# Kernel tuning notes

Hardware: AMD Instinct MI355X
Metric: run time of the kernel (lower is better)

The kernel has to match this reference:

```python
import jax, jax.numpy as jnp
import numpy as np

B = 256; L = 512; PRED = 96; DVARS = 21
P = 16; STRIDE = 16
N = (L - P) // STRIDE + 1      # 32 patches
DM = P * P                     # d_model = 256
K = 5                          # DctAtt low-freq coeffs
EPS_BN = 1e-5


def _dct_mats(n_len):
    # torch_dct DCT-II / DCT-III as dense matrices (exact same scaling as torch_dct)
    n = jnp.arange(n_len, dtype=jnp.float32)
    C = jnp.cos(jnp.pi * (2.0 * n[None, :] + 1.0) * n[:, None] / (2.0 * n_len))  # (k, m)
    D2 = 2.0 * C                                  # dct(x, norm=None):  X = x @ D2.T
    w0 = jnp.where(n == 0, 0.5, 1.0)
    D3 = (C.T * w0[None, :]) / n_len              # idct(X, norm=None): x = X @ D3.T
    rL = jnp.sqrt(jnp.asarray(n_len, jnp.float32))
    s_ortho = jnp.where(n == 0, 0.5 / rL, 0.5 * jnp.sqrt(2.0) / rL)  # unnorm -> ortho scale
    return D2, D3, s_ortho


def _bn(x, g, b):
    # BatchNorm1d, training-mode batch stats (biased var), x: (B, C, Lc)
    m = jnp.mean(x, axis=(0, 2), keepdims=True)
    v = jnp.var(x, axis=(0, 2), keepdims=True)
    return g[None, :, None] * (x - m) * jax.lax.rsqrt(v + EPS_BN) + b[None, :, None]


def _gelu(x):
    return jax.nn.gelu(x, approximate=False)  # torch nn.GELU default = exact erf


def setup_inputs():
    key = jax.random.key(0)
    ks = jax.random.split(key, 24)
    r = lambda i, shp, s=0.02: jax.random.normal(ks[i], shp, jnp.float32) * s
    return dict(
        x=jax.random.normal(ks[0], (B, L, DVARS), jnp.float32),
        w_dct=r(1, (DVARS,), 0.2), b_dct=r(2, (DVARS,), 0.02),
        W_embed=r(3, (P, DM), 0.05), b_embed=r(4, (DM,), 0.02),
        W_linres=r(5, (N * DM, PRED), 0.01), b_linres=r(6, (PRED,), 0.02),
        W_dres=r(7, (DM, P), 0.05), b_dres=r(8, (P,), 0.02),
        w_dc=r(9, (N, P), 0.1), b_dc=r(10, (N,), 0.02),
        w_dc1=r(11, (N, 3), 0.2), b_dc1=r(12, (N,), 0.02),
        g_dctnorm=jnp.ones((DVARS,), jnp.float32), b_dctnorm=jnp.zeros((DVARS,), jnp.float32),
        g_patchnorm=jnp.ones((N,), jnp.float32), b_patchnorm=jnp.zeros((N,), jnp.float32),
        g_depthnorm=jnp.ones((N,), jnp.float32), b_depthnorm=jnp.zeros((N,), jnp.float32),
        thr_p=jnp.array([0.3], jnp.float32),
        W_m1=r(13, (L, PRED), 0.02), b_m1=r(14, (PRED,), 0.02),
        W_m2=r(15, (PRED, PRED), 0.05), b_m2=r(16, (PRED,), 0.02),
        a_dw_w=r(17, (K,), 0.2), a_dw_b=r(18, (), 0.02),
        a_cw=jnp.float32(1.0) + r(19, (), 0.1), a_cb=r(20, (), 0.02),
        a_g=jnp.ones((), jnp.float32), a_b=jnp.zeros((), jnp.float32),
    )


def reference(x, w_dct, b_dct, W_embed, b_embed, W_linres, b_linres,
              W_dres, b_dres, w_dc, b_dc, w_dc1, b_dc1,
              g_dctnorm, b_dctnorm, g_patchnorm, b_patchnorm,
              g_depthnorm, b_depthnorm, thr_p,
              W_m1, b_m1, W_m2, b_m2,
              a_dw_w, a_dw_b, a_cw, a_cb, a_g, a_b):
    Bx = x.shape[0]
    D2, D3, s_ortho = _dct_mats(L)
    xT = jnp.transpose(x, (0, 2, 1))                       # (B,D,L)
    # dctConv = depthwise 1x1 conv => per-channel scale+bias (same layer reused twice)
    x_res = xT * w_dct[:, None] + b_dct[:, None]
    z_dct = xT @ D2.T                                      # dct(norm=None)
    # adaptive_high_freq_mask
    energy = jnp.sum(z_dct * z_dct, axis=-1)               # (B,D)
    med = jnp.median(energy, axis=1, keepdims=True)
    norm_e = energy / (med + 1e-6)
    thr = jnp.quantile(norm_e, thr_p[0])                   # global quantile over all elems
    mask = (norm_e > thr).astype(x.dtype)[..., None]       # broadcasts over freq axis
    z = (z_dct * mask) * w_dct[:, None] + b_dct[:, None]
    z = _gelu(z)
    z = _bn(z, g_dctnorm, b_dctnorm)
    z1 = z @ D3.T + x_res                                  # idct + residual, (B,D,L)
    # patchify (unfold)
    idx = jnp.arange(N)[:, None] * STRIDE + jnp.arange(P)[None, :]
    zp = xT[..., idx].reshape(Bx * DVARS, N, P)            # (BD,N,P)
    z_p = zp @ W_embed + b_embed                           # (BD,N,DM)
    z_res = jnp.transpose(z_p.reshape(Bx, DVARS, N * DM) @ W_linres + b_linres, (0, 2, 1))
    res = z_p @ W_dres + b_dres                            # (BD,N,P)
    # depth_conv: depthwise conv, kernel=P, stride=P over DM=P*P
    zd = jnp.einsum('bnqp,np->bnq', z_p.reshape(Bx * DVARS, N, P, P), w_dc) + b_dc[:, None]
    zd = _bn(zd + res, g_patchnorm, b_patchnorm)
    z2 = _gelu(zd)
    # depth_conv1: depthwise k=3 pad=1
    zpad = jnp.pad(z2, ((0, 0), (0, 0), (1, 1)))
    zc = (w_dc1[:, 0, None] * zpad[..., :-2] + w_dc1[:, 1, None] * zpad[..., 1:-1]
          + w_dc1[:, 2, None] * zpad[..., 2:]) + b_dc1[:, None]
    zc = _bn(zc, g_depthnorm, b_depthnorm)
    zc = _gelu(zc) + z2
    z2f = zc.reshape(Bx, DVARS, N * P)                     # (B,D,L)
    # DctAtt on z1*z2f (low-freq pick + dwConv(k=5,stride=5) + BN(1) + GELU + 1x1 + softmax)
    prod = z1 * z2f
    low = (prod @ D2.T[:, :K]) * s_ortho[:K]               # ortho DCT, first K coeffs (B,D,K)
    att = low @ a_dw_w + a_dw_b                            # (B,D)
    m = jnp.mean(att); v = jnp.var(att)
    att = a_g * (att - m) * jax.lax.rsqrt(v + EPS_BN) + a_b
    att = _gelu(att)
    att1 = jax.nn.softmax(att * a_cw + a_cb, axis=-1)[..., None]  # (B,D,1)
    zsum = z1 * att1 + z2f * (1.0 - att1)
    z_mlp = _gelu(zsum @ W_m1 + b_m1) @ W_m2 + b_m2        # Mlp, (B,D,PRED)
    return z_res + jnp.transpose(z_mlp, (0, 2, 1))         # (B,PRED,D)
```

## Files before the change

### kernel.cpp

```cpp
#include <hip/hip_runtime.h>
#include <hip/hip_bf16.h>

#define B_    256
#define L_    512
#define DV    21
#define NROW  5376
#define NP    32
#define PP    16
#define PRED_ 96

static const size_t OFF_XT    = 0;
static const size_t OFF_ZA    = 2752512;
static const size_t OFF_Z1    = 5505024;
static const size_t OFF_ZCP   = 8257536;
static const size_t OFF_D2    = 11010048;
static const size_t OFF_D3    = 11272192;
static const size_t OFF_M     = 11534336;
static const size_t OFF_TN    = 11583488;
static const size_t OFF_TB    = 11591680;
static const size_t OFF_C     = 11592192;
static const size_t OFF_EN    = 11592320;
static const size_t OFF_NORM  = 11597696;
static const size_t OFF_ATT   = 11603072;
static const size_t OFF_ATT1  = 11608448;
static const size_t OFF_STAT  = 11613824;
static const size_t OFF_ABD   = 11614080;
static const size_t OFF_ABP   = 11614144;
static const size_t OFF_ABDEP = 11614208;
static const size_t OFF_FLAG  = 11614272;
static const size_t OFF_STG   = 11614336;

static const int S_WDCT=0, S_BDCT=24, S_WE=48, S_BE=4144, S_WL=4400, S_BL=790832,
  S_WD=790928, S_BDRES=795024, S_WDC=795040, S_BDC=795552, S_WDC1=795584, S_BDC1=795680,
  S_GD=795712, S_BDN=795736, S_GP=795760, S_BP=795792, S_GDEP=795824, S_BDEP=795856,
  S_THR=795888, S_WM1=795892, S_BM1=845044, S_WM2=845140, S_BM2=854356,
  S_ADWW=854452, S_ADWB=854460, S_ACW=854464, S_ACB=854468, S_AG=854472, S_AB2=854476;

struct Ptrs { const void* p[30]; };

typedef __attribute__((ext_vector_type(8))) short bf16x8;
typedef __attribute__((ext_vector_type(4))) float f32x4;

__device__ __forceinline__ float bf2f(unsigned short h){
  unsigned u = ((unsigned)h) << 16;
  return __uint_as_float(u);
}
__device__ __forceinline__ short f2b(float f){
  unsigned u = __float_as_uint(f);
  u = (u + 0x7FFFu + ((u >> 16) & 1u)) >> 16;
  return (short)u;
}
__device__ __forceinline__ float gelu_f(float x){ return 0.5f*x*(1.0f+erff(x*0.70710678118654752440f)); }

__global__ void k_init(const unsigned* __restrict__ gones, float* __restrict__ stat,
                       float* __restrict__ c, float* __restrict__ M, int* __restrict__ flag){
  if (blockIdx.x == 0){
    stat[threadIdx.x] = 0.0f;
    if (threadIdx.x < 128) c[threadIdx.x] = 0.0f;
    if (threadIdx.x == 0) *flag = (gones[0] == 0x3F800000u) ? 1 : 0;
  } else {
    M[(blockIdx.x-1)*256 + threadIdx.x] = 0.0f;
  }
}

__global__ __launch_bounds__(256) void k_stage(Ptrs ptrs, float* __restrict__ dst, const int* __restrict__ flag){
  const int cnt[29] = {21,21,4096,256,786432,96,4096,16,512,32,96,32,21,21,32,32,32,32,1,49152,96,9216,96,5,1,1,1,1,1};
  const int off[29] = {S_WDCT,S_BDCT,S_WE,S_BE,S_WL,S_BL,S_WD,S_BDRES,S_WDC,S_BDC,S_WDC1,S_BDC1,
                       S_GD,S_BDN,S_GP,S_BP,S_GDEP,S_BDEP,S_THR,S_WM1,S_BM1,S_WM2,S_BM2,
                       S_ADWW,S_ADWB,S_ACW,S_ACB,S_AG,S_AB2};
  int mode = *flag;
  int gid = blockIdx.x*256 + threadIdx.x;
  int a = -1, loc = 0, base = 0;
  #pragma unroll
  for (int i = 0; i < 29; i++){
    if (a < 0 && gid < base + cnt[i]){ a = i; loc = gid - base; }
    base += cnt[i];
  }
  if (a < 0) return;
  const void* s = ptrs.p[a+1];
  float v = mode ? ((const float*)s)[loc] : bf2f(((const unsigned short*)s)[loc]);
  dst[off[a] + loc] = v;
}

__global__ __launch_bounds__(256) void k_transpose(const void* __restrict__ x, float* __restrict__ xt,
                                                   const int* __restrict__ flag){
  __shared__ float xs[128*DV];
  int mode = *flag;
  int b = blockIdx.x >> 2, ch = blockIdx.x & 3;
  int l0 = ch*128;
  size_t base = (size_t)b*(L_*DV) + (size_t)l0*DV;
  if (mode){
    const float* xp = (const float*)x + base;
    for (int i = threadIdx.x; i < 128*DV; i += 256) xs[i] = xp[i];
  } else {
    const unsigned short* xp = (const unsigned short*)x + base;
    for (int i = threadIdx.x; i < 128*DV; i += 256) xs[i] = bf2f(xp[i]);
  }
  __syncthreads();
  for (int i = threadIdx.x; i < 128*DV; i += 256){
    int d = i >> 7, l = i & 127;
    xt[((size_t)b*DV + d)*512 + l0 + l] = xs[l*DV + d];
  }
}

__global__ __launch_bounds__(256) void k_dctmats(unsigned short* __restrict__ D2h,
    unsigned short* __restrict__ D2l, unsigned short* __restrict__ D3h,
    const float* __restrict__ S, float* __restrict__ dvec){
  int i = blockIdx.x*256 + threadIdx.x;
  int kk = i >> 9, m = i & 511;
  const float PIo = 3.14159265358979323846f / 1024.0f;
  int a = ((2*m+1)*kk) & 2047;
  float v = 2.0f * cosf(PIo * (float)a);
  short hi = f2b(v);
  float lo = v - bf2f((unsigned short)hi);
  D2h[i] = (unsigned short)hi;
  D2l[i] = (unsigned short)f2b(lo);
  int l = kk, k = m;
  int a2 = ((2*l+1)*k) & 2047;
  float w0 = (k==0) ? 0.5f : 1.0f;
  D3h[i] = (unsigned short)f2b(cosf(PIo * (float)a2) * w0 * (1.0f/512.0f));
  if (i < 512){
    const float rs = 22.627416997969522f;
    float s = 0.f;
    #pragma unroll
    for (int k5 = 0; k5 < 5; k5++){
      float sk = ((k5 == 0) ? 0.5f : 0.70710678118654752440f) / rs;
      int a5 = ((2*i+1)*k5) & 2047;
      s += 2.0f * cosf(PIo * (float)a5) * sk * S[S_ADWW + k5];
    }
    dvec[i] = s;
  }
}

__global__ __launch_bounds__(256) void k_foldM(const float* __restrict__ S, float* __restrict__ M){
  const float* We = S + S_WE;  const float* Wl = S + S_WL;
  int gid = blockIdx.x*256 + threadIdx.x;
  int l = gid/96, p = gid - l*96;
  int n = l>>4, q = l&15;
  int j0 = blockIdx.y*32;
  float acc = 0.f;
  #pragma unroll 8
  for (int j = j0; j < j0+32; j++) acc += We[q*256+j] * Wl[(size_t)(n*256+j)*96 + p];
  atomicAdd(&M[gid], acc);
}

__global__ __launch_bounds__(256) void k_foldC(const float* __restrict__ S, float* __restrict__ c){
  const float* be = S + S_BE;  const float* Wl = S + S_WL;  const float* bl = S + S_BL;
  int t = threadIdx.x;
  int rp = t >> 7, p = t & 127;
  if (p >= 96) return;
  float acc = 0.f;
  int J0 = blockIdx.x*64;
  for (int j = 0; j < 64; j += 2){
    int J = J0 + j + rp;
    acc += be[J & 255] * Wl[(size_t)J*96 + p];
  }
  if (blockIdx.x == 0 && rp == 0) acc += bl[p];
  atomicAdd(&c[p], acc);
}

__global__ __launch_bounds__(256) void k_foldTn(const float* __restrict__ S,
    float* __restrict__ Tn, float* __restrict__ tb){
  __shared__ float WeS[4096];
  __shared__ float WdS[4096];
  __shared__ float wdcS[16];
  __shared__ float beS[256];
  __shared__ float bdresS[16];
  int n = blockIdx.x, tid = threadIdx.x;
  for (int i = tid; i < 4096; i += 256){ WeS[i] = S[S_WE+i]; WdS[i] = S[S_WD+i]; }
  beS[tid & 255] = S[S_BE + (tid & 255)];
  if (tid < 16){ wdcS[tid] = S[S_WDC + n*16 + tid]; bdresS[tid] = S[S_BDRES + tid]; }
  __syncthreads();
  int q2 = tid>>4, q = tid&15;
  float R = 0.f;
  for (int j = 0; j < 256; j++) R += WeS[q2*256+j] * WdS[j*16+q];
  float G = 0.f;
  #pragma unroll
  for (int p = 0; p < 16; p++) G += WeS[q2*256 + q*16 + p] * wdcS[p];
  Tn[n*256 + q2*16 + q] = R + G;
  if (tid < 16){
    float rb = bdresS[tid];
    for (int j = 0; j < 256; j++) rb += beS[j] * WdS[j*16+tid];
    float gb = S[S_BDC + n];
    #pragma unroll
    for (int p = 0; p < 16; p++) gb += beS[tid*16+p] * wdcS[p];
    tb[n*16+tid] = rb + gb;
  }
}

__global__ __launch_bounds__(256) void k_gemm0(
    const float* __restrict__ A, const unsigned short* __restrict__ Bh16,
    const unsigned short* __restrict__ Bl16, float* __restrict__ C,
    float* __restrict__ e_part){
  __shared__ short Ahi[64*40];
  __shared__ short Alo[64*40];
  __shared__ short Bhi[64*40];
  __shared__ short Blo[64*40];
  int tid = threadIdx.x;
  int rowBase = blockIdx.y*64, colBase = blockIdx.x*64;
  int srow = tid>>2, seg = tid&3;
  int r = rowBase + srow;
  int wave = tid>>6, lane = tid&63;
  int m = lane&15, quad = lane>>4;
  f32x4 acc[4] = {};
  for (int k0 = 0; k0 < 512; k0 += 32){
    float4 a0 = *(const float4*)(A + (size_t)r*512 + k0 + seg*8);
    float4 a1 = *(const float4*)(A + (size_t)r*512 + k0 + seg*8 + 4);
    bf16x8 ah, al;
    {
      float av[8] = {a0.x,a0.y,a0.z,a0.w,a1.x,a1.y,a1.z,a1.w};
      #pragma unroll
      for (int j = 0; j < 8; j++){
        short h = f2b(av[j]);
        ah[j] = h;
        al[j] = f2b(av[j] - bf2f((unsigned short)h));
      }
    }
    *(bf16x8*)(Ahi + srow*40 + seg*8) = ah;
    *(bf16x8*)(Alo + srow*40 + seg*8) = al;
    *(bf16x8*)(Bhi + srow*40 + seg*8) = *(const bf16x8*)(Bh16 + (size_t)(colBase+srow)*512 + k0 + seg*8);
    *(bf16x8*)(Blo + srow*40 + seg*8) = *(const bf16x8*)(Bl16 + (size_t)(colBase+srow)*512 + k0 + seg*8);
    __syncthreads();
    bf16x8 afh = *(bf16x8*)(Ahi + (wave*16 + m)*40 + quad*8);
    bf16x8 afl = *(bf16x8*)(Alo + (wave*16 + m)*40 + quad*8);
    #pragma unroll
    for (int t = 0; t < 4; t++){
      bf16x8 bfh = *(bf16x8*)(Bhi + (t*16 + m)*40 + quad*8);
      bf16x8 bfl = *(bf16x8*)(Blo + (t*16 + m)*40 + quad*8);
      acc[t] = __builtin_amdgcn_mfma_f32_16x16x32_bf16(afh, bfh, acc[t], 0, 0, 0);
      acc[t] = __builtin_amdgcn_mfma_f32_16x16x32_bf16(afh, bfl, acc[t], 0, 0, 0);
      acc[t] = __builtin_amdgcn_mfma_f32_16x16x32_bf16(afl, bfh, acc[t], 0, 0, 0);
      acc[t] = __builtin_amdgcn_mfma_f32_16x16x32_bf16(afl, bfl, acc[t], 0, 0, 0);
    }
    __syncthreads();
  }
  float es[4] = {};
  #pragma unroll
  for (int t = 0; t < 4; t++){
    #pragma unroll
    for (int i = 0; i < 4; i++){
      int rr = rowBase + wave*16 + quad*4 + i;
      int cc = colBase + t*16 + m;
      float v = acc[t][i];
      C[(size_t)rr*512 + cc] = v;
      es[i] += v*v;
    }
  }
  #pragma unroll
  for (int off = 1; off < 16; off <<= 1){
    #pragma unroll
    for (int i = 0; i < 4; i++) es[i] += __shfl_xor(es[i], off);
  }
  if (m == 0){
    #pragma unroll
    for (int i = 0; i < 4; i++){
      int rr = rowBase + wave*16 + quad*4 + i;
      e_part[rr*8 + blockIdx.x] = es[i];
    }
  }
}

__global__ __launch_bounds__(256) void k_ered(const float* __restrict__ e_part, float* __restrict__ e){
  int r = blockIdx.x*256 + threadIdx.x;
  float s = 0.f;
  #pragma unroll
  for (int j = 0; j < 8; j++) s += e_part[r*8 + j];
  e[r] = s;
}

template<int MODE>
__global__ __launch_bounds__(256) void k_gemm_mf(
    const float* __restrict__ A, const float* __restrict__ A2,
    const unsigned short* __restrict__ Bg,
    float* __restrict__ C, const float* __restrict__ ab, const float* __restrict__ xt,
    const float* __restrict__ wdct, const float* __restrict__ bdct, int Cstride){
  __shared__ short Ah[64*40];
  __shared__ short Bh[64*40];
  int tid = threadIdx.x;
  int rowBase = blockIdx.y*64, colBase = blockIdx.x*64;
  int srow = tid>>2, seg = tid&3;
  int r = rowBase + srow;
  float alpha = 1.f, beta = 0.f;
  bool useXt = false;
  if (MODE == 1){ int d = r % DV; alpha = ab[2*d]; beta = ab[2*d+1]; }
  if (MODE == 3){ if (blockIdx.x < 2) alpha = ab[r]; else useXt = true; }
  int wave = tid>>6, lane = tid&63;
  int m = lane&15, quad = lane>>4;
  f32x4 acc[4] = {};
  const float* Ap = (MODE == 3 && useXt) ? xt : A;
  for (int k0 = 0; k0 < 512; k0 += 32){
    float4 a0 = *(const float4*)(Ap + (size_t)r*512 + k0 + seg*8);
    float4 a1 = *(const float4*)(Ap + (size_t)r*512 + k0 + seg*8 + 4);
    if (MODE == 1){
      a0.x = alpha*a0.x+beta; a0.y = alpha*a0.y+beta; a0.z = alpha*a0.z+beta; a0.w = alpha*a0.w+beta;
      a1.x = alpha*a1.x+beta; a1.y = alpha*a1.y+beta; a1.z = alpha*a1.z+beta; a1.w = alpha*a1.w+beta;
    }
    if (MODE == 3 && !useXt){
      float4 c0 = *(const float4*)(A2 + (size_t)r*512 + k0 + seg*8);
      float4 c1 = *(const float4*)(A2 + (size_t)r*512 + k0 + seg*8 + 4);
      float om = 1.0f - alpha;
      a0.x = alpha*a0.x + om*c0.x; a0.y = alpha*a0.y + om*c0.y;
      a0.z = alpha*a0.z + om*c0.z; a0.w = alpha*a0.w + om*c0.w;
      a1.x = alpha*a1.x + om*c1.x; a1.y = alpha*a1.y + om*c1.y;
      a1.z = alpha*a1.z + om*c1.z; a1.w = alpha*a1.w + om*c1.w;
    }
    bf16x8 av;
    av[0]=f2b(a0.x); av[1]=f2b(a0.y); av[2]=f2b(a0.z); av[3]=f2b(a0.w);
    av[4]=f2b(a1.x); av[5]=f2b(a1.y); av[6]=f2b(a1.z); av[7]=f2b(a1.w);
    *(bf16x8*)(Ah + srow*40 + seg*8) = av;
    bf16x8 bv = *(const bf16x8*)(Bg + (size_t)(colBase+srow)*512 + k0 + seg*8);
    *(bf16x8*)(Bh + srow*40 + seg*8) = bv;
    __syncthreads();
    bf16x8 af = *(bf16x8*)(Ah + (wave*16 + m)*40 + quad*8);
    #pragma unroll
    for (int t = 0; t < 4; t++){
      bf16x8 bf = *(bf16x8*)(Bh + (t*16 + m)*40 + quad*8);
      acc[t] = __builtin_amdgcn_mfma_f32_16x16x32_bf16(af, bf, acc[t], 0, 0, 0);
    }
    __syncthreads();
  }
  #pragma unroll
  for (int t = 0; t < 4; t++){
    #pragma unroll
    for (int i = 0; i < 4; i++){
      int rr = rowBase + wave*16 + quad*4 + i;
      int cc = colBase + t*16 + m;
      float v = acc[t][i];
      if (MODE == 1){
        int d = rr % DV;
        v += xt[(size_t)rr*512 + cc]*wdct[d] + bdct[d];
      }
      C[(size_t)rr*Cstride + cc] = v;
    }
  }
}

__global__ __launch_bounds__(256) void k_med(const float* __restrict__ e, float* __restrict__ norm){
  int b = threadIdx.x;
  float v[DV];
  for (int d = 0; d < DV; d++) v[d] = e[b*DV + d];
  float med = 0.f;
  for (int i = 0; i < DV; i++){
    int rk = 0;
    for (int j = 0; j < DV; j++) rk += (v[j] < v[i]) || (v[j] == v[i] && j < i);
    if (rk == 10) med = v[i];
  }
  float den = med + 1e-6f;
  for (int d = 0; d < DV; d++) norm[b*DV + d] = v[d] / den;
}

__global__ __launch_bounds__(256) void k_rank(const float* __restrict__ norm,
    const float* __restrict__ thrv, float* __restrict__ stat){
  int tid = threadIdx.x;
  int cand = tid >> 4, part = tid & 15;
  int idx = blockIdx.x*16 + cand;
  float val = norm[idx];
  int cnt = 0;
  int j0 = part*336;
  for (int j = j0; j < j0 + 336; ++j){
    float v = norm[j];
    cnt += (v < val) || (v == val && j < idx);
  }
  __shared__ int sc[16][17];
  sc[cand][part] = cnt;
  __syncthreads();
  if (part == 0){
    int rank = 0;
    #pragma unroll
    for (int i = 0; i < 16; i++) rank += sc[cand][i];
    float q = thrv[0];
    float pos = q * 5375.0f;
    int i0 = (int)floorf(pos);
    int i1 = (i0 + 1 > 5375) ? 5375 : i0 + 1;
    if (rank == i0) stat[200] = val;
    if (rank == i1) stat[201] = val;
  }
}

__global__ __launch_bounds__(256) void k_maskgelu(float* __restrict__ zA, const float* __restrict__ norm,
    const float* __restrict__ stat, const float* __restrict__ thrv,
    const float* __restrict__ wdct, const float* __restrict__ bdct,
    float* __restrict__ part){
  int r = blockIdx.x, tid = threadIdx.x;
  int d = r % DV, brow = r / DV;
  float q = thrv[0];
  float pos = q * 5375.0f; float f = pos - floorf(pos);
  float thr = stat[200] + (stat[201] - stat[200]) * f;
  float mask = norm[r] > thr ? 1.0f : 0.0f;
  float w = wdct[d], b = bdct[d];
  float s = 0.f, s2 = 0.f;
  for (int i = tid; i < 512; i += 256){
    float v = zA[(size_t)r*512 + i] * mask * w + b;
    float g = gelu_f(v);
    zA[(size_t)r*512 + i] = g;
    s += g; s2 += g*g;
  }
  for (int off = 32; off; off >>= 1){ s += __shfl_down(s, off); s2 += __shfl_down(s2, off); }
  __shared__ float wsum[4][2];
  int wv = tid >> 6;
  if ((tid & 63) == 0){ wsum[wv][0] = s; wsum[wv][1] = s2; }
  __syncthreads();
  if (tid == 0){
    float S  = wsum[0][0]+wsum[1][0]+wsum[2][0]+wsum[3][0];
    float S2 = wsum[0][1]+wsum[1][1]+wsum[2][1]+wsum[3][1];
    part[(2*d)*256 + brow] = S;
    part[(2*d+1)*256 + brow] = S2;
  }
}

__global__ __launch_bounds__(256) void k_bnfin2(const float* __restrict__ part, int P,
    const float* __restrict__ g, const float* __restrict__ b, float count, float* __restrict__ ab){
  int c = blockIdx.x, tid = threadIdx.x;
  const float* ps = part + (size_t)(2*c)*P;
  const float* pq = part + (size_t)(2*c+1)*P;
  float s = 0.f, s2 = 0.f;
  for (int i = tid; i < P; i += 256){ s += ps[i]; s2 += pq[i]; }
  for (int off = 32; off; off >>= 1){ s += __shfl_down(s, off); s2 += __shfl_down(s2, off); }
  __shared__ float ws[4][2];
  if ((tid & 63) == 0){ ws[tid>>6][0] = s; ws[tid>>6][1] = s2; }
  __syncthreads();
  if (tid == 0){
    float S1 = ws[0][0]+ws[1][0]+ws[2][0]+ws[3][0];
    float S2 = ws[0][1]+ws[1][1]+ws[2][1]+ws[3][1];
    float mean = S1 / count;
    float var  = S2 / count - mean*mean;
    float al = g[c] * rsqrtf(var + 1e-5f);
    float be = b[c] - mean * al;
    ab[2*c] = al; ab[2*c+1] = be;
  }
}

__global__ __launch_bounds__(256) void k_patch(const float* __restrict__ xt, const float* __restrict__ Tn,
    const float* __restrict__ tb, float* __restrict__ t, float* __restrict__ part){
  int blk = blockIdx.x, tid = threadIdx.x;
  int n0 = tid >> 4, qq = tid & 15;
  int n1 = n0 + 16;
  float T0[16], T1[16];
  #pragma unroll
  for (int q2 = 0; q2 < 16; q2++){
    T0[q2] = Tn[n0*256 + q2*16 + qq];
    T1[q2] = Tn[n1*256 + q2*16 + qq];
  }
  float tb0 = tb[n0*16 + qq], tb1 = tb[n1*16 + qq];
  float s0 = 0.f, q0 = 0.f, s1 = 0.f, q1 = 0.f;
  #pragma unroll
  for (int rr = 0; rr < 4; rr++){
    int r = blk*4 + rr;
    float x0 = xt[(size_t)r*512 + tid];
    float x1 = xt[(size_t)r*512 + tid + 256];
    float a0 = tb0, a1 = tb1;
    #pragma unroll
    for (int q2 = 0; q2 < 16; q2++){
      a0 += __shfl(x0, q2, 16) * T0[q2];
      a1 += __shfl(x1, q2, 16) * T1[q2];
    }
    t[(size_t)r*512 + tid] = a0;       s0 += a0; q0 += a0*a0;
    t[(size_t)r*512 + tid + 256] = a1; s1 += a1; q1 += a1*a1;
  }
  #pragma unroll
  for (int off = 1; off < 16; off <<= 1){
    s0 += __shfl_xor(s0, off); q0 += __shfl_xor(q0, off);
    s1 += __shfl_xor(s1, off); q1 += __shfl_xor(q1, off);
  }
  if (qq == 0){
    part[(2*n0)*1344 + blk] = s0; part[(2*n0+1)*1344 + blk] = q0;
    part[(2*n1)*1344 + blk] = s1; part[(2*n1+1)*1344 + blk] = q1;
  }
}

__global__ __launch_bounds__(256) void k_z2(float* __restrict__ t, float* __restrict__ zcp,
    const float* __restrict__ abp, const float* __restrict__ wdc1,
    const float* __restrict__ bdc1, float* __restrict__ part){
  int blk = blockIdx.x, tid = threadIdx.x;
  int n0 = tid >> 4, qq = tid & 15;
  int n1 = n0 + 16;
  float al0 = abp[2*n0], be0 = abp[2*n0+1], al1 = abp[2*n1], be1 = abp[2*n1+1];
  float w00 = wdc1[n0*3], w01 = wdc1[n0*3+1], w02 = wdc1[n0*3+2], bb0 = bdc1[n0];
  float w10 = wdc1[n1*3], w11 = wdc1[n1*3+1], w12 = wdc1[n1*3+2], bb1 = bdc1[n1];
  float s0 = 0.f, q0 = 0.f, s1 = 0.f, q1 = 0.f;
  #pragma unroll
  for (int rr = 0; rr < 4; rr++){
    int r = blk*4 + rr;
    float v0 = t[(size_t)r*512 + tid];
    float v1 = t[(size_t)r*512 + tid + 256];
    float z0  = gelu_f(al0*v0 + be0);
    float z1v = gelu_f(al1*v1 + be1);
    float l0 = __shfl_up(z0, 1, 16);    if (qq == 0)  l0 = 0.f;
    float r0 = __shfl_down(z0, 1, 16);  if (qq == 15) r0 = 0.f;
    float l1 = __shfl_up(z1v, 1, 16);   if (qq == 0)  l1 = 0.f;
    float r1 = __shfl_down(z1v, 1, 16); if (qq == 15) r1 = 0.f;
    float cv0 = w00*l0 + w01*z0  + w02*r0 + bb0;
    float cv1 = w10*l1 + w11*z1v + w12*r1 + bb1;
    zcp[(size_t)r*512 + tid] = cv0;       t[(size_t)r*512 + tid] = z0;
    zcp[(size_t)r*512 + tid + 256] = cv1; t[(size_t)r*512 + tid + 256] = z1v;
    s0 += cv0; q0 += cv0*cv0; s1 += cv1; q1 += cv1*cv1;
  }
  #pragma unroll
  for (int off = 1; off < 16; off <<= 1){
    s0 += __shfl_xor(s0, off); q0 += __shfl_xor(q0, off);
    s1 += __shfl_xor(s1, off); q1 += __shfl_xor(q1, off);
  }
  if (qq == 0){
    part[(2*n0)*1344 + blk] = s0; part[(2*n0+1)*1344 + blk] = q0;
    part[(2*n1)*1344 + blk] = s1; part[(2*n1+1)*1344 + blk] = q1;
  }
}

__global__ __launch_bounds__(256) void k_z2fatt(float* __restrict__ zcp, const float* __restrict__ z2,
    const float* __restrict__ ab, const float* __restrict__ z1,
    const float* __restrict__ dvec, float* __restrict__ att){
  int r = blockIdx.x, tid = threadIdx.x;
  size_t base = (size_t)r*512;
  float s = 0.f;
  #pragma unroll
  for (int h = 0; h < 2; h++){
    int idx = tid + h*256;
    int n = (idx >> 4) & 31;
    float v = gelu_f(ab[2*n]*zcp[base+idx] + ab[2*n+1]) + z2[base+idx];
    zcp[base+idx] = v;
    s += z1[base+idx] * v * dvec[idx];
  }
  for (int off = 32; off; off >>= 1) s += __shfl_down(s, off);
  __shared__ float ws[4];
  if ((tid & 63) == 0) ws[tid>>6] = s;
  __syncthreads();
  if (tid == 0) att[r] = ws[0]+ws[1]+ws[2]+ws[3];
}

__global__ __launch_bounds__(256) void k_attfin(const float* __restrict__ att, const float* __restrict__ S,
                                                float* __restrict__ att1){
  __shared__ float ws[4][2];
  int tid = threadIdx.x;
  float s = 0.f, s2 = 0.f;
  for (int i = tid; i < NROW; i += 256){ float a = att[i]; s += a; s2 += a*a; }
  for (int off = 32; off; off >>= 1){ s += __shfl_down(s, off); s2 += __shfl_down(s2, off); }
  if ((tid & 63) == 0){ ws[tid>>6][0] = s; ws[tid>>6][1] = s2; }
  __syncthreads();
  float S1 = ws[0][0]+ws[1][0]+ws[2][0]+ws[3][0];
  float S2 = ws[0][1]+ws[1][1]+ws[2][1]+ws[3][1];
  float mean = S1 / 5376.0f;
  float var  = S2 / 5376.0f - mean*mean;
  float al = S[S_AG] * rsqrtf(var + 1e-5f);
  float bb = S[S_AB2];
  float cw = S[S_ACW], cb2 = S[S_ACB];
  int b = tid;
  float v[DV]; float mx = -1e30f;
  for (int d = 0; d < DV; d++){
    float a = att[b*DV + d];
    a = gelu_f(al*(a - mean) + bb);
    a = a*cw + cb2;
    v[d] = a; mx = fmaxf(mx, a);
  }
  float ss = 0.f;
  for (int d = 0; d < DV; d++){ v[d] = expf(v[d] - mx); ss += v[d]; }
  float inv = 1.0f / ss;
  for (int d = 0; d < DV; d++) att1[b*DV + d] = v[d] * inv;
}

__global__ __launch_bounds__(256) void k_bcat(const float* __restrict__ Wm1, const float* __restrict__ M,
                                              unsigned short* __restrict__ Bt){
  int i = blockIdx.x*256 + threadIdx.x;
  int c = i >> 9, m = i & 511;
  float v = 0.f;
  if (c < 96) v = Wm1[m*96 + c];
  else if (c >= 128 && c < 224) v = M[m*96 + (c - 128)];
  Bt[i] = (unsigned short)f2b(v);
}

__global__ __launch_bounds__(256) void k_out(const float* __restrict__ Hcat, const float* __restrict__ c,
    const float* __restrict__ S, void* __restrict__ outv, const int* __restrict__ flag){
  const float* bm1 = S + S_BM1;
  const float* Wm2 = S + S_WM2;
  const float* bm2 = S + S_BM2;
  __shared__ float W2s[96*96];
  __shared__ float Hs[16][100];
  int blk = blockIdx.x, tid = threadIdx.x;
  int r0 = blk*16;
  for (int i = tid; i < 96*96; i += 256) W2s[i] = Wm2[i];
  for (int i = tid; i < 16*96; i += 256){
    int rr = i / 96, col = i - rr*96;
    Hs[rr][col] = gelu_f(Hcat[(size_t)(r0+rr)*256 + col] + bm1[col]);
  }
  __syncthreads();
  int rr = tid >> 4, c0 = (tid & 15)*6;
  float acc[6] = {};
  for (int k = 0; k < 96; k++){
    float h = Hs[rr][k];
    #pragma unroll
    for (int j = 0; j < 6; j++) acc[j] += h * W2s[k*96 + c0 + j];
  }
  int r = r0 + rr;
  int b = r / DV, d = r - b*DV;
  int mode = *flag;
  #pragma unroll
  for (int j = 0; j < 6; j++){
    int p = c0 + j;
    float val = Hcat[(size_t)r*256 + 128 + p] + c[p] + acc[j] + bm2[p];
    size_t oi = ((size_t)b*96 + p)*DV + d;
    if (mode) ((float*)outv)[oi] = val;
    else ((__hip_bfloat16*)outv)[oi] = __float2bfloat16(val);
  }
}

extern "C" void kernel_launch(void* const* d_in, const int* in_sizes, int n_in,
                              void* d_out, int out_size, void* d_ws, size_t ws_size,
                              hipStream_t stream) {
  float* w = (float*)d_ws;
  float* xt   = w + OFF_XT;
  float* zA   = w + OFF_ZA;
  float* z1   = w + OFF_Z1;
  float* zcp  = w + OFF_ZCP;
  unsigned short* D2h = (unsigned short*)(w + OFF_D2);
  unsigned short* D2l = (unsigned short*)(w + OFF_D2 + 131072);
  unsigned short* D3h = (unsigned short*)(w + OFF_D3);
  float* Mb   = w + OFF_M;
  float* Tn   = w + OFF_TN;
  float* tb   = w + OFF_TB;
  float* cb   = w + OFF_C;
  float* en   = w + OFF_EN;
  float* nrm  = w + OFF_NORM;
  float* att  = w + OFF_ATT;
  float* att1 = w + OFF_ATT1;
  float* dvec = w + OFF_ATT1;
  float* stat = w + OFF_STAT;
  float* abd  = w + OFF_ABD;
  float* abp  = w + OFF_ABP;
  float* abdep= w + OFF_ABDEP;
  int*   flag = (int*)(w + OFF_FLAG);
  float* S    = w + OFF_STG;
  float* Hcat = zA;
  unsigned short* BcatTh = (unsigned short*)(zA + 1500000);
  float* partA  = w + OFF_D2;
  float* e_part = w + OFF_D3 + 131072;
  float* partB  = w + OFF_D3 + 131072;

  Ptrs ptrs;
  for (int i = 0; i < 30; i++) ptrs.p[i] = d_in[i];

  k_init<<<193, 256, 0, stream>>>((const unsigned*)d_in[13], stat, cb, Mb, flag);
  k_stage<<<3338, 256, 0, stream>>>(ptrs, S, flag);
  k_transpose<<<1024, 256, 0, stream>>>(d_in[0], xt, flag);
  k_dctmats<<<1024, 256, 0, stream>>>(D2h, D2l, D3h, S, dvec);
  k_foldM<<<dim3(192, 8), 256, 0, stream>>>(S, Mb);
  k_foldC<<<128, 256, 0, stream>>>(S, cb);
  k_foldTn<<<32, 256, 0, stream>>>(S, Tn, tb);

  k_gemm0<<<dim3(8,84), 256, 0, stream>>>(xt, D2h, D2l, zA, e_part);
  k_ered<<<21, 256, 0, stream>>>(e_part, en);
  k_med<<<1, 256, 0, stream>>>(en, nrm);
  k_rank<<<336, 256, 0, stream>>>(nrm, S+S_THR, stat);
  k_maskgelu<<<NROW, 256, 0, stream>>>(zA, nrm, stat, S+S_THR, S+S_WDCT, S+S_BDCT, partA);
  k_bnfin2<<<DV, 256, 0, stream>>>(partA, 256, S+S_GD, S+S_BDN, 131072.0f, abd);
  k_gemm_mf<1><<<dim3(8,84), 256, 0, stream>>>(zA, nullptr, D3h, z1, abd, xt, S+S_WDCT, S+S_BDCT, 512);

  k_patch<<<NROW/4, 256, 0, stream>>>(xt, Tn, tb, zA, partA);
  k_bnfin2<<<NP, 256, 0, stream>>>(partA, 1344, S+S_GP, S+S_BP, 86016.0f, abp);
  k_z2<<<NROW/4, 256, 0, stream>>>(zA, zcp, abp, S+S_WDC1, S+S_BDC1, partB);
  k_bnfin2<<<NP, 256, 0, stream>>>(partB, 1344, S+S_GDEP, S+S_BDEP, 86016.0f, abdep);
  k_z2fatt<<<NROW, 256, 0, stream>>>(zcp, zA, abdep, z1, dvec, att);
  k_attfin<<<1, 256, 0, stream>>>(att, S, att1);

  k_bcat<<<512, 256, 0, stream>>>(S+S_WM1, Mb, BcatTh);
  k_gemm_mf<3><<<dim3(4,84), 256, 0, stream>>>(z1, zcp, BcatTh, Hcat, att1, xt, nullptr, nullptr, 256);
  k_out<<<NROW/16, 256, 0, stream>>>(Hcat, cb, S, d_out, flag);
}
```

Baseline: 318.9 us.

## Merge independent kernels into block-range-dispatched launches to cut launch count

Folds many small kernels into a few launches that pick their role by block-index range: setup (stage, transpose, DCT matrices, init), fold (M, c, Tn), a mega kernel running GEMM0, patch embed and Bcat build side by side, and several mid kernels that fuse the BN reductions with the following elementwise passes. It gives the patch path its own buffers so it no longer aliases zA, which lets the independent branches run concurrently. The aim is to remove launch overhead and serialization between small independent stages. The cost is heterogeneous blocks sharing one launch and extra workspace.

```diff
diff --git a/kernel.cpp b/kernel.cpp
--- a/kernel.cpp
+++ b/kernel.cpp
@@ -29,6 +29,12 @@
 static const size_t OFF_ABDEP = 11614208;
 static const size_t OFF_FLAG  = 11614272;
 static const size_t OFF_STG   = 11614336;
+static const size_t OFF_T     = 12468816;
+static const size_t OFF_PARTP = 15221328;
+static const size_t OFF_PARTD = 15307344;
+static const size_t OFF_EPART = 15393360;
+static const size_t OFF_PARTM = 15436368;
+static const size_t OFF_BCAT  = 15447120;
 
 static const int S_WDCT=0, S_BDCT=24, S_WE=48, S_BE=4144, S_WL=4400, S_BL=790832,
   S_WD=790928, S_BDRES=795024, S_WDC=795040, S_BDC=795552, S_WDC1=795584, S_BDC1=795680,
@@ -52,220 +58,420 @@
 }
 __device__ __forceinline__ float gelu_f(float x){ return 0.5f*x*(1.0f+erff(x*0.70710678118654752440f)); }
 
-__global__ void k_init(const unsigned* __restrict__ gones, float* __restrict__ stat,
-                       float* __restrict__ c, float* __restrict__ M, int* __restrict__ flag){
-  if (blockIdx.x == 0){
-    stat[threadIdx.x] = 0.0f;
-    if (threadIdx.x < 128) c[threadIdx.x] = 0.0f;
-    if (threadIdx.x == 0) *flag = (gones[0] == 0x3F800000u) ? 1 : 0;
+__global__ __launch_bounds__(256) void k_setup(Ptrs ptrs, float* __restrict__ W,
+    float* __restrict__ xt, unsigned short* __restrict__ D2h, unsigned short* __restrict__ D2l,
+    unsigned short* __restrict__ D3h, float* __restrict__ dvec){
+  int b = blockIdx.x, tid = threadIdx.x;
+  int mode = (((const unsigned*)ptrs.p[13])[0] == 0x3F800000u) ? 1 : 0;
+  float* S = W + OFF_STG;
+  if (b < 3338){
+    const int cnt[29] = {21,21,4096,256,786432,96,4096,16,512,32,96,32,21,21,32,32,32,32,1,49152,96,9216,96,5,1,1,1,1,1};
+    const int off[29] = {S_WDCT,S_BDCT,S_WE,S_BE,S_WL,S_BL,S_WD,S_BDRES,S_WDC,S_BDC,S_WDC1,S_BDC1,
+                         S_GD,S_BDN,S_GP,S_BP,S_GDEP,S_BDEP,S_THR,S_WM1,S_BM1,S_WM2,S_BM2,
+                         S_ADWW,S_ADWB,S_ACW,S_ACB,S_AG,S_AB2};
+    int gid = b*256 + tid;
+    int a = -1, loc = 0, base = 0;
+    #pragma unroll
+    for (int i = 0; i < 29; i++){
+      if (a < 0 && gid < base + cnt[i]){ a = i; loc = gid - base; }
+      base += cnt[i];
+    }
+    if (a < 0) return;
+    const void* s = ptrs.p[a+1];
+    S[off[a] + loc] = mode ? ((const float*)s)[loc] : bf2f(((const unsigned short*)s)[loc]);
+  } else if (b < 4362){
+    __shared__ float xs[128*DV];
+    int b2 = b - 3338;
+    int bb = b2 >> 2, ch = b2 & 3;
+    int l0 = ch*128;
+    size_t base = (size_t)bb*(L_*DV) + (size_t)l0*DV;
+    if (mode){
+      const float* xp = (const float*)ptrs.p[0] + base;
+      for (int i = tid; i < 128*DV; i += 256) xs[i] = xp[i];
+    } else {
+      const unsigned short* xp = (const unsigned short*)ptrs.p[0] + base;
+      for (int i = tid; i < 128*DV; i += 256) xs[i] = bf2f(xp[i]);
+    }
+    __syncthreads();
+    for (int i = tid; i < 128*DV; i += 256){
+      int d = i >> 7, l = i & 127;
+      xt[((size_t)bb*DV + d)*512 + l0 + l] = xs[l*DV + d];
+    }
+  } else if (b < 5386){
+    int i = (b - 4362)*256 + tid;
+    int kk = i >> 9, m = i & 511;
+    const float PIo = 3.14159265358979323846f / 1024.0f;
+    int a = ((2*m+1)*kk) & 2047;
+    float v = 2.0f * cosf(PIo * (float)a);
+    short hi = f2b(v);
+    D2h[i] = (unsigned short)hi;
+    D2l[i] = (unsigned short)f2b(v - bf2f((unsigned short)hi));
+    int a2 = ((2*kk+1)*m) & 2047;
+    float w0 = (m==0) ? 0.5f : 1.0f;
+    D3h[i] = (unsigned short)f2b(cosf(PIo * (float)a2) * w0 * (1.0f/512.0f));
+    if (i < 512){
+      const float rs = 22.627416997969522f;
+      const void* aw = ptrs.p[24];
+      float s = 0.f;
+      #pragma unroll
+      for (int k5 = 0; k5 < 5; k5++){
+        float awk = mode ? ((const float*)aw)[k5] : bf2f(((const unsigned short*)aw)[k5]);
+        float sk = ((k5 == 0) ? 0.5f : 0.70710678118654752440f) / rs;
+        int a5 = ((2*i+1)*k5) & 2047;
+        s += 2.0f * cosf(PIo * (float)a5) * sk * awk;
+      }
+      dvec[i] = s;
+    }
   } else {
-    M[(blockIdx.x-1)*256 + threadIdx.x] = 0.0f;
-  }
-}
-
-__global__ __launch_bounds__(256) void k_stage(Ptrs ptrs, float* __restrict__ dst, const int* __restrict__ flag){
-  const int cnt[29] = {21,21,4096,256,786432,96,4096,16,512,32,96,32,21,21,32,32,32,32,1,49152,96,9216,96,5,1,1,1,1,1};
-  const int off[29] = {S_WDCT,S_BDCT,S_WE,S_BE,S_WL,S_BL,S_WD,S_BDRES,S_WDC,S_BDC,S_WDC1,S_BDC1,
-                       S_GD,S_BDN,S_GP,S_BP,S_GDEP,S_BDEP,S_THR,S_WM1,S_BM1,S_WM2,S_BM2,
-                       S_ADWW,S_ADWB,S_ACW,S_ACB,S_AG,S_AB2};
-  int mode = *flag;
-  int gid = blockIdx.x*256 + threadIdx.x;
-  int a = -1, loc = 0, base = 0;
-  #pragma unroll
-  for (int i = 0; i < 29; i++){
-    if (a < 0 && gid < base + cnt[i]){ a = i; loc = gid - base; }
-    base += cnt[i];
-  }
-  if (a < 0) return;
-  const void* s = ptrs.p[a+1];
-  float v = mode ? ((const float*)s)[loc] : bf2f(((const unsigned short*)s)[loc]);
-  dst[off[a] + loc] = v;
-}
-
-__global__ __launch_bounds__(256) void k_transpose(const void* __restrict__ x, float* __restrict__ xt,
-                                                   const int* __restrict__ flag){
-  __shared__ float xs[128*DV];
-  int mode = *flag;
-  int b = blockIdx.x >> 2, ch = blockIdx.x & 3;
-  int l0 = ch*128;
-  size_t base = (size_t)b*(L_*DV) + (size_t)l0*DV;
-  if (mode){
-    const float* xp = (const float*)x + base;
-    for (int i = threadIdx.x; i < 128*DV; i += 256) xs[i] = xp[i];
+    int bz = b - 5386;
+    if (bz == 0){
+      W[OFF_STAT + tid] = 0.0f;
+      if (tid < 128) W[OFF_C + tid] = 0.0f;
+      if (tid == 0) *(int*)(W + OFF_FLAG) = mode;
+    } else {
+      W[OFF_M + (size_t)(bz-1)*256 + tid] = 0.0f;
+    }
+  }
+}
+
+__global__ __launch_bounds__(256) void k_fold(const float* __restrict__ S,
+    float* __restrict__ M, float* __restrict__ c, float* __restrict__ Tn, float* __restrict__ tb){
+  int b = blockIdx.x, tid = threadIdx.x;
+  if (b < 1536){
+    const float* We = S + S_WE;  const float* Wl = S + S_WL;
+    int y = b / 192, xb = b - y*192;
+    int gid = xb*256 + tid;
+    int l = gid/96, p = gid - l*96;
+    int n = l>>4, q = l&15;
+    int j0 = y*32;
+    float acc = 0.f;
+    #pragma unroll 8
+    for (int j = j0; j < j0+32; j++) acc += We[q*256+j] * Wl[(size_t)(n*256+j)*96 + p];
+    atomicAdd(&M[gid], acc);
+  } else if (b < 1664){
+    const float* be = S + S_BE;  const float* Wl = S + S_WL;  const float* bl = S + S_BL;
+    int blkC = b - 1536;
+    int rp = tid >> 7, p = tid & 127;
+    if (p >= 96) return;
+    float acc = 0.f;
+    int J0 = blkC*64;
+    for (int j = 0; j < 64; j += 2){
+      int J = J0 + j + rp;
+      acc += be[J & 255] * Wl[(size_t)J*96 + p];
+    }
+    if (blkC == 0 && rp == 0) acc += bl[p];
+    atomicAdd(&c[p], acc);
   } else {
-    const unsigned short* xp = (const unsigned short*)x + base;
-    for (int i = threadIdx.x; i < 128*DV; i += 256) xs[i] = bf2f(xp[i]);
-  }
+    __shared__ float WeS[4096];
+    __shared__ float WdS[4096];
+    __shared__ float wdcS[16];
+    __shared__ float beS[256];
+    __shared__ float bdresS[16];
+    int n = b - 1664;
+    for (int i = tid; i < 4096; i += 256){ WeS[i] = S[S_WE+i]; WdS[i] = S[S_WD+i]; }
+    beS[tid & 255] = S[S_BE + (tid & 255)];
+    if (tid < 16){ wdcS[tid] = S[S_WDC + n*16 + tid]; bdresS[tid] = S[S_BDRES + tid]; }
+    __syncthreads();
+    int q2 = tid>>4, q = tid&15;
+    float R = 0.f;
+    for (int j = 0; j < 256; j++) R += WeS[q2*256+j] * WdS[j*16+q];
+    float G = 0.f;
+    #pragma unroll
+    for (int p = 0; p < 16; p++) G += WeS[q2*256 + q*16 + p] * wdcS[p];
+    Tn[n*256 + q2*16 + q] = R + G;
+    if (tid < 16){
+      float rb = bdresS[tid];
+      for (int j = 0; j < 256; j++) rb += beS[j] * WdS[j*16+tid];
+      float gb = S[S_BDC + n];
+      #pragma unroll
+      for (int p = 0; p < 16; p++) gb += beS[tid*16+p] * wdcS[p];
+      tb[n*16+tid] = rb + gb;
+    }
+  }
+}
+
+__global__ __launch_bounds__(256) void k_mega(
+    const float* __restrict__ xt, const unsigned short* __restrict__ Bh16,
+    const unsigned short* __restrict__ Bl16, float* __restrict__ C,
+    float* __restrict__ e_part, const int* __restrict__ flag,
+    const float* __restrict__ Tn, const float* __restrict__ tb,
+    float* __restrict__ t, float* __restrict__ partP,
+    const float* __restrict__ S, const float* __restrict__ M, unsigned short* __restrict__ Bt){
+  int b = blockIdx.x, tid = threadIdx.x;
+  if (b < 672){
+    __shared__ short Ahi[64*40];
+    __shared__ short Alo[64*40];
+    __shared__ short Bhi[64*40];
+    __shared__ short Blo[64*40];
+    int mode = *flag;
+    int bx = b & 7, by = b >> 3;
+    int rowBase = by*64, colBase = bx*64;
+    int srow = tid>>2, seg = tid&3;
+    int r = rowBase + srow;
+    int wave = tid>>6, lane = tid&63;
+    int m = lane&15, quad = lane>>4;
+    f32x4 acc[4] = {};
+    for (int k0 = 0; k0 < 512; k0 += 32){
+      float4 a0 = *(const float4*)(xt + (size_t)r*512 + k0 + seg*8);
+      float4 a1 = *(const float4*)(xt + (size_t)r*512 + k0 + seg*8 + 4);
+      bf16x8 ah;
+      float av[8] = {a0.x,a0.y,a0.z,a0.w,a1.x,a1.y,a1.z,a1.w};
+      #pragma unroll
+      for (int j = 0; j < 8; j++) ah[j] = f2b(av[j]);
+      *(bf16x8*)(Ahi + srow*40 + seg*8) = ah;
+      if (mode){
+        bf16x8 al;
+        #pragma unroll
+        for (int j = 0; j < 8; j++) al[j] = f2b(av[j] - bf2f((unsigned short)ah[j]));
+        *(bf16x8*)(Alo + srow*40 + seg*8) = al;
+      }
+      *(bf16x8*)(Bhi + srow*40 + seg*8) = *(const bf16x8*)(Bh16 + (size_t)(colBase+srow)*512 + k0 + seg*8);
+      *(bf16x8*)(Blo + srow*40 + seg*8) = *(const bf16x8*)(Bl16 + (size_t)(colBase+srow)*512 + k0 + seg*8);
+      __syncthreads();
+      bf16x8 afh = *(bf16x8*)(Ahi + (wave*16 + m)*40 + quad*8);
+      #pragma unroll
+      for (int tt = 0; tt < 4; tt++){
+        bf16x8 bfh = *(bf16x8*)(Bhi + (tt*16 + m)*40 + quad*8);
+        bf16x8 bfl = *(bf16x8*)(Blo + (tt*16 + m)*40 + quad*8);
+        acc[tt] = __builtin_amdgcn_mfma_f32_16x16x32_bf16(afh, bfh, acc[tt], 0, 0, 0);
+        acc[tt] = __builtin_amdgcn_mfma_f32_16x16x32_bf16(afh, bfl, acc[tt], 0, 0, 0);
+      }
+      if (mode){
+        bf16x8 afl = *(bf16x8*)(Alo + (wave*16 + m)*40 + quad*8);
+        #pragma unroll
+        for (int tt = 0; tt < 4; tt++){
+          bf16x8 bfh = *(bf16x8*)(Bhi + (tt*16 + m)*40 + quad*8);
+          bf16x8 bfl = *(bf16x8*)(Blo + (tt*16 + m)*40 + quad*8);
+          acc[tt] = __builtin_amdgcn_mfma_f32_16x16x32_bf16(afl, bfh, acc[tt], 0, 0, 0);
+          acc[tt] = __builtin_amdgcn_mfma_f32_16x16x32_bf16(afl, bfl, acc[tt], 0, 0, 0);
+        }
+      }
+      __syncthreads();
+    }
+    float es[4] = {};
+    #pragma unroll
+    for (int tt = 0; tt < 4; tt++){
+      #pragma unroll
+      for (int i = 0; i < 4; i++){
+        int rr = rowBase + wave*16 + quad*4 + i;
+        int cc = colBase + tt*16 + m;
+        float v = acc[tt][i];
+        C[(size_t)rr*512 + cc] = v;
+        es[i] += v*v;
+      }
+    }
+    #pragma unroll
+    for (int off = 1; off < 16; off <<= 1){
+      #pragma unroll
+      for (int i = 0; i < 4; i++) es[i] += __shfl_xor(es[i], off);
+    }
+    if (m == 0){
+      #pragma unroll
+      for (int i = 0; i < 4; i++){
+        int rr = rowBase + wave*16 + quad*4 + i;
+        e_part[rr*8 + bx] = es[i];
+      }
+    }
+  } else if (b < 2016){
+    int blk = b - 672;
+    int n0 = tid >> 4, qq = tid & 15;
+    int n1 = n0 + 16;
+    float T0[16], T1[16];
+    #pragma unroll
+    for (int q2 = 0; q2 < 16; q2++){
+      T0[q2] = Tn[n0*256 + q2*16 + qq];
+      T1[q2] = Tn[n1*256 + q2*16 + qq];
+    }
+    float tb0 = tb[n0*16 + qq], tb1 = tb[n1*16 + qq];
+    float s0 = 0.f, q0 = 0.f, s1 = 0.f, q1 = 0.f;
+    #pragma unroll
+    for (int rr = 0; rr < 4; rr++){
+      int r = blk*4 + rr;
+      float x0 = xt[(size_t)r*512 + tid];
+      float x1 = xt[(size_t)r*512 + tid + 256];
+      float a0 = tb0, a1 = tb1;
+      #pragma unroll
+      for (int q2 = 0; q2 < 16; q2++){
+        a0 += __shfl(x0, q2, 16) * T0[q2];
+        a1 += __shfl(x1, q2, 16) * T1[q2];
+      }
+      t[(size_t)r*512 + tid] = a0;       s0 += a0; q0 += a0*a0;
+      t[(size_t)r*512 + tid + 256] = a1; s1 += a1; q1 += a1*a1;
+    }
+    #pragma unroll
+    for (int off = 1; off < 16; off <<= 1){
+      s0 += __shfl_xor(s0, off); q0 += __shfl_xor(q0, off);
+      s1 += __shfl_xor(s1, off); q1 += __shfl_xor(q1, off);
+    }
+    if (qq == 0){
+      partP[(2*n0)*1344 + blk] = s0; partP[(2*n0+1)*1344 + blk] = q0;
+      partP[(2*n1)*1344 + blk] = s1; partP[(2*n1+1)*1344 + blk] = q1;
+    }
+  } else {
+    int i = (b - 2016)*256 + tid;
+    int cc = i >> 9, m = i & 511;
+    float v = 0.f;
+    if (cc < 96) v = S[S_WM1 + m*96 + cc];
+    else if (cc >= 128 && cc < 224) v = M[m*96 + (cc - 128)];
+    Bt[i] = (unsigned short)f2b(v);
+  }
+}
+
+__device__ __forceinline__ void dev_bnfin(const float* part, int P, const float* g,
+    const float* bb, float count, float* ab, int c, int tid){
+  const float* ps = part + (size_t)(2*c)*P;
+  const float* pq = part + (size_t)(2*c+1)*P;
+  float s = 0.f, s2 = 0.f;
+  for (int i = tid; i < P; i += 256){ s += ps[i]; s2 += pq[i]; }
+  for (int off = 32; off; off >>= 1){ s += __shfl_down(s, off); s2 += __shfl_down(s2, off); }
+  __shared__ float ws[4][2];
+  if ((tid & 63) == 0){ ws[tid>>6][0] = s; ws[tid>>6][1] = s2; }
   __syncthreads();
-  for (int i = threadIdx.x; i < 128*DV; i += 256){
-    int d = i >> 7, l = i & 127;
-    xt[((size_t)b*DV + d)*512 + l0 + l] = xs[l*DV + d];
-  }
-}
-
-__global__ __launch_bounds__(256) void k_dctmats(unsigned short* __restrict__ D2h,
-    unsigned short* __restrict__ D2l, unsigned short* __restrict__ D3h,
-    const float* __restrict__ S, float* __restrict__ dvec){
-  int i = blockIdx.x*256 + threadIdx.x;
-  int kk = i >> 9, m = i & 511;
-  const float PIo = 3.14159265358979323846f / 1024.0f;
-  int a = ((2*m+1)*kk) & 2047;
-  float v = 2.0f * cosf(PIo * (float)a);
-  short hi = f2b(v);
-  float lo = v - bf2f((unsigned short)hi);
-  D2h[i] = (unsigned short)hi;
-  D2l[i] = (unsigned short)f2b(lo);
-  int l = kk, k = m;
-  int a2 = ((2*l+1)*k) & 2047;
-  float w0 = (k==0) ? 0.5f : 1.0f;
-  D3h[i] = (unsigned short)f2b(cosf(PIo * (float)a2) * w0 * (1.0f/512.0f));
-  if (i < 512){
-    const float rs = 22.627416997969522f;
-    float s = 0.f;
-    #pragma unroll
-    for (int k5 = 0; k5 < 5; k5++){
-      float sk = ((k5 == 0) ? 0.5f : 0.70710678118654752440f) / rs;
-      int a5 = ((2*i+1)*k5) & 2047;
-      s += 2.0f * cosf(PIo * (float)a5) * sk * S[S_ADWW + k5];
-    }
-    dvec[i] = s;
-  }
-}
-
-__global__ __launch_bounds__(256) void k_foldM(const float* __restrict__ S, float* __restrict__ M){
-  const float* We = S + S_WE;  const float* Wl = S + S_WL;
-  int gid = blockIdx.x*256 + threadIdx.x;
-  int l = gid/96, p = gid - l*96;
-  int n = l>>4, q = l&15;
-  int j0 = blockIdx.y*32;
-  float acc = 0.f;
-  #pragma unroll 8
-  for (int j = j0; j < j0+32; j++) acc += We[q*256+j] * Wl[(size_t)(n*256+j)*96 + p];
-  atomicAdd(&M[gid], acc);
-}
-
-__global__ __launch_bounds__(256) void k_foldC(const float* __restrict__ S, float* __restrict__ c){
-  const float* be = S + S_BE;  const float* Wl = S + S_WL;  const float* bl = S + S_BL;
-  int t = threadIdx.x;
-  int rp = t >> 7, p = t & 127;
-  if (p >= 96) return;
-  float acc = 0.f;
-  int J0 = blockIdx.x*64;
-  for (int j = 0; j < 64; j += 2){
-    int J = J0 + j + rp;
-    acc += be[J & 255] * Wl[(size_t)J*96 + p];
-  }
-  if (blockIdx.x == 0 && rp == 0) acc += bl[p];
-  atomicAdd(&c[p], acc);
-}
-
-__global__ __launch_bounds__(256) void k_foldTn(const float* __restrict__ S,
-    float* __restrict__ Tn, float* __restrict__ tb){
-  __shared__ float WeS[4096];
-  __shared__ float WdS[4096];
-  __shared__ float wdcS[16];
-  __shared__ float beS[256];
-  __shared__ float bdresS[16];
-  int n = blockIdx.x, tid = threadIdx.x;
-  for (int i = tid; i < 4096; i += 256){ WeS[i] = S[S_WE+i]; WdS[i] = S[S_WD+i]; }
-  beS[tid & 255] = S[S_BE + (tid & 255)];
-  if (tid < 16){ wdcS[tid] = S[S_WDC + n*16 + tid]; bdresS[tid] = S[S_BDRES + tid]; }
-  __syncthreads();
-  int q2 = tid>>4, q = tid&15;
-  float R = 0.f;
-  for (int j = 0; j < 256; j++) R += WeS[q2*256+j] * WdS[j*16+q];
-  float G = 0.f;
-  #pragma unroll
-  for (int p = 0; p < 16; p++) G += WeS[q2*256 + q*16 + p] * wdcS[p];
-  Tn[n*256 + q2*16 + q] = R + G;
-  if (tid < 16){
-    float rb = bdresS[tid];
-    for (int j = 0; j < 256; j++) rb += beS[j] * WdS[j*16+tid];
-    float gb = S[S_BDC + n];
-    #pragma unroll
-    for (int p = 0; p < 16; p++) gb += beS[tid*16+p] * wdcS[p];
-    tb[n*16+tid] = rb + gb;
-  }
-}
-
-__global__ __launch_bounds__(256) void k_gemm0(
-    const float* __restrict__ A, const unsigned short* __restrict__ Bh16,
-    const unsigned short* __restrict__ Bl16, float* __restrict__ C,
-    float* __restrict__ e_part){
-  __shared__ short Ahi[64*40];
-  __shared__ short Alo[64*40];
-  __shared__ short Bhi[64*40];
-  __shared__ short Blo[64*40];
-  int tid = threadIdx.x;
-  int rowBase = blockIdx.y*64, colBase = blockIdx.x*64;
-  int srow = tid>>2, seg = tid&3;
-  int r = rowBase + srow;
-  int wave = tid>>6, lane = tid&63;
-  int m = lane&15, quad = lane>>4;
-  f32x4 acc[4] = {};
-  for (int k0 = 0; k0 < 512; k0 += 32){
-    float4 a0 = *(const float4*)(A + (size_t)r*512 + k0 + seg*8);
-    float4 a1 = *(const float4*)(A + (size_t)r*512 + k0 + seg*8 + 4);
-    bf16x8 ah, al;
-    {
-      float av[8] = {a0.x,a0.y,a0.z,a0.w,a1.x,a1.y,a1.z,a1.w};
-      #pragma unroll
-      for (int j = 0; j < 8; j++){
-        short h = f2b(av[j]);
-        ah[j] = h;
-        al[j] = f2b(av[j] - bf2f((unsigned short)h));
-      }
-    }
-    *(bf16x8*)(Ahi + srow*40 + seg*8) = ah;
-    *(bf16x8*)(Alo + srow*40 + seg*8) = al;
-    *(bf16x8*)(Bhi + srow*40 + seg*8) = *(const bf16x8*)(Bh16 + (size_t)(colBase+srow)*512 + k0 + seg*8);
-    *(bf16x8*)(Blo + srow*40 + seg*8) = *(const bf16x8*)(Bl16 + (size_t)(colBase+srow)*512 + k0 + seg*8);
+  if (tid == 0){
+    float S1 = ws[0][0]+ws[1][0]+ws[2][0]+ws[3][0];
+    float S2 = ws[0][1]+ws[1][1]+ws[2][1]+ws[3][1];
+    float mean = S1 / count;
+    float var  = S2 / count - mean*mean;
+    float al = g[c] * rsqrtf(var + 1e-5f);
+    float be = bb[c] - mean * al;
+    ab[2*c] = al; ab[2*c+1] = be;
+  }
+}
+
+__global__ __launch_bounds__(256) void k_mid1(const float* __restrict__ e_part,
+    float* __restrict__ en, float* __restrict__ norm,
+    const float* __restrict__ partP, const float* __restrict__ S, float* __restrict__ abp){
+  int b = blockIdx.x, tid = threadIdx.x;
+  if (b == 0){
+    for (int r = tid; r < NROW; r += 256){
+      float s = 0.f;
+      #pragma unroll
+      for (int j = 0; j < 8; j++) s += e_part[r*8 + j];
+      en[r] = s;
+    }
     __syncthreads();
-    bf16x8 afh = *(bf16x8*)(Ahi + (wave*16 + m)*40 + quad*8);
-    bf16x8 afl = *(bf16x8*)(Alo + (wave*16 + m)*40 + quad*8);
-    #pragma unroll
-    for (int t = 0; t < 4; t++){
-      bf16x8 bfh = *(bf16x8*)(Bhi + (t*16 + m)*40 + quad*8);
-      bf16x8 bfl = *(bf16x8*)(Blo + (t*16 + m)*40 + quad*8);
-      acc[t] = __builtin_amdgcn_mfma_f32_16x16x32_bf16(afh, bfh, acc[t], 0, 0, 0);
-      acc[t] = __builtin_amdgcn_mfma_f32_16x16x32_bf16(afh, bfl, acc[t], 0, 0, 0);
-      acc[t] = __builtin_amdgcn_mfma_f32_16x16x32_bf16(afl, bfh, acc[t], 0, 0, 0);
-      acc[t] = __builtin_amdgcn_mfma_f32_16x16x32_bf16(afl, bfl, acc[t], 0, 0, 0);
-    }
+    int bb = tid;
+    float v[DV];
+    for (int d = 0; d < DV; d++) v[d] = en[bb*DV + d];
+    float med = 0.f;
+    for (int i = 0; i < DV; i++){
+      int rk = 0;
+      for (int j = 0; j < DV; j++) rk += (v[j] < v[i]) || (v[j] == v[i] && j < i);
+      if (rk == 10) med = v[i];
+    }
+    float den = med + 1e-6f;
+    for (int d = 0; d < DV; d++) norm[bb*DV + d] = v[d] / den;
+  } else {
+    dev_bnfin(partP, 1344, S + S_GP, S + S_BP, 86016.0f, abp, b - 1, tid);
+  }
+}
+
+__global__ __launch_bounds__(256) void k_mid2(const float* __restrict__ norm,
+    const float* __restrict__ S, float* __restrict__ stat,
+    float* __restrict__ t, float* __restrict__ zcp,
+    const float* __restrict__ abp, float* __restrict__ partD){
+  int b = blockIdx.x, tid = threadIdx.x;
+  if (b < 336){
+    int cand = tid >> 4, part = tid & 15;
+    int idx = b*16 + cand;
+    float val = norm[idx];
+    int cnt = 0;
+    int j0 = part*336;
+    for (int j = j0; j < j0 + 336; ++j){
+      float v = norm[j];
+      cnt += (v < val) || (v == val && j < idx);
+    }
+    __shared__ int sc[16][17];
+    sc[cand][part] = cnt;
     __syncthreads();
-  }
-  float es[4] = {};
-  #pragma unroll
-  for (int t = 0; t < 4; t++){
-    #pragma unroll
-    for (int i = 0; i < 4; i++){
-      int rr = rowBase + wave*16 + quad*4 + i;
-      int cc = colBase + t*16 + m;
-      float v = acc[t][i];
-      C[(size_t)rr*512 + cc] = v;
-      es[i] += v*v;
-    }
-  }
-  #pragma unroll
-  for (int off = 1; off < 16; off <<= 1){
-    #pragma unroll
-    for (int i = 0; i < 4; i++) es[i] += __shfl_xor(es[i], off);
-  }
-  if (m == 0){
-    #pragma unroll
-    for (int i = 0; i < 4; i++){
-      int rr = rowBase + wave*16 + quad*4 + i;
-      e_part[rr*8 + blockIdx.x] = es[i];
-    }
-  }
-}
-
-__global__ __launch_bounds__(256) void k_ered(const float* __restrict__ e_part, float* __restrict__ e){
-  int r = blockIdx.x*256 + threadIdx.x;
-  float s = 0.f;
-  #pragma unroll
-  for (int j = 0; j < 8; j++) s += e_part[r*8 + j];
-  e[r] = s;
+    if (part == 0){
+      int rank = 0;
+      #pragma unroll
+      for (int i = 0; i < 16; i++) rank += sc[cand][i];
+      float q = S[S_THR];
+      float pos = q * 5375.0f;
+      int i0 = (int)floorf(pos);
+      int i1 = (i0 + 1 > 5375) ? 5375 : i0 + 1;
+      if (rank == i0) stat[200] = val;
+      if (rank == i1) stat[201] = val;
+    }
+  } else {
+    int blk = b - 336;
+    const float* wdc1 = S + S_WDC1;
+    const float* bdc1 = S + S_BDC1;
+    int n0 = tid >> 4, qq = tid & 15;
+    int n1 = n0 + 16;
+    float al0 = abp[2*n0], be0 = abp[2*n0+1], al1 = abp[2*n1], be1 = abp[2*n1+1];
+    float w00 = wdc1[n0*3], w01 = wdc1[n0*3+1], w02 = wdc1[n0*3+2], bb0 = bdc1[n0];
+    float w10 = wdc1[n1*3], w11 = wdc1[n1*3+1], w12 = wdc1[n1*3+2], bb1 = bdc1[n1];
+    float s0 = 0.f, q0 = 0.f, s1 = 0.f, q1 = 0.f;
+    #pragma unroll
+    for (int rr = 0; rr < 4; rr++){
+      int r = blk*4 + rr;
+      float v0 = t[(size_t)r*512 + tid];
+      float v1 = t[(size_t)r*512 + tid + 256];
+      float z0  = gelu_f(al0*v0 + be0);
+      float z1v = gelu_f(al1*v1 + be1);
+      float l0 = __shfl_up(z0, 1, 16);    if (qq == 0)  l0 = 0.f;
+      float r0 = __shfl_down(z0, 1, 16);  if (qq == 15) r0 = 0.f;
+      float l1 = __shfl_up(z1v, 1, 16);   if (qq == 0)  l1 = 0.f;
+      float r1 = __shfl_down(z1v, 1, 16); if (qq == 15) r1 = 0.f;
+      float cv0 = w00*l0 + w01*z0  + w02*r0 + bb0;
+      float cv1 = w10*l1 + w11*z1v + w12*r1 + bb1;
+      zcp[(size_t)r*512 + tid] = cv0;       t[(size_t)r*512 + tid] = z0;
+      zcp[(size_t)r*512 + tid + 256] = cv1; t[(size_t)r*512 + tid + 256] = z1v;
+      s0 += cv0; q0 += cv0*cv0; s1 += cv1; q1 += cv1*cv1;
+    }
+    #pragma unroll
+    for (int off = 1; off < 16; off <<= 1){
+      s0 += __shfl_xor(s0, off); q0 += __shfl_xor(q0, off);
+      s1 += __shfl_xor(s1, off); q1 += __shfl_xor(q1, off);
+    }
+    if (qq == 0){
+      partD[(2*n0)*1344 + blk] = s0; partD[(2*n0+1)*1344 + blk] = q0;
+      partD[(2*n1)*1344 + blk] = s1; partD[(2*n1+1)*1344 + blk] = q1;
+    }
+  }
+}
+
+__global__ __launch_bounds__(256) void k_mid3(float* __restrict__ zA, const float* __restrict__ norm,
+    const float* __restrict__ stat, const float* __restrict__ S,
+    float* __restrict__ partM, const float* __restrict__ partD, float* __restrict__ abdep){
+  int b = blockIdx.x, tid = threadIdx.x;
+  if (b < NROW){
+    int r = b;
+    int d = r % DV, brow = r / DV;
+    float q = S[S_THR];
+    float pos = q * 5375.0f; float f = pos - floorf(pos);
+    float thr = stat[200] + (stat[201] - stat[200]) * f;
+    float mask = norm[r] > thr ? 1.0f : 0.0f;
+    float w = S[S_WDCT + d], bb = S[S_BDCT + d];
+    float s = 0.f, s2 = 0.f;
+    for (int i = tid; i < 512; i += 256){
+      float v = zA[(size_t)r*512 + i] * mask * w + bb;
+      float g = gelu_f(v);
+      zA[(size_t)r*512 + i] = g;
+      s += g; s2 += g*g;
+    }
+    for (int off = 32; off; off >>= 1){ s += __shfl_down(s, off); s2 += __shfl_down(s2, off); }
+    __shared__ float wsum[4][2];
+    int wv = tid >> 6;
+    if ((tid & 63) == 0){ wsum[wv][0] = s; wsum[wv][1] = s2; }
+    __syncthreads();
+    if (tid == 0){
+      float SS  = wsum[0][0]+wsum[1][0]+wsum[2][0]+wsum[3][0];
+      float SS2 = wsum[0][1]+wsum[1][1]+wsum[2][1]+wsum[3][1];
+      partM[(2*d)*256 + brow] = SS;
+      partM[(2*d+1)*256 + brow] = SS2;
+    }
+  } else {
+    dev_bnfin(partD, 1344, S + S_GDEP, S + S_BDEP, 86016.0f, abdep, b - NROW, tid);
+  }
+}
+
+__global__ __launch_bounds__(256) void k_mid4(const float* __restrict__ partM,
+    const float* __restrict__ S, float* __restrict__ abd){
+  dev_bnfin(partM, 256, S + S_GD, S + S_BDN, 131072.0f, abd, blockIdx.x, threadIdx.x);
 }
 
 template<int MODE>
@@ -335,177 +541,6 @@
   }
 }
 
-__global__ __launch_bounds__(256) void k_med(const float* __restrict__ e, float* __restrict__ norm){
-  int b = threadIdx.x;
-  float v[DV];
-  for (int d = 0; d < DV; d++) v[d] = e[b*DV + d];
-  float med = 0.f;
-  for (int i = 0; i < DV; i++){
-    int rk = 0;
-    for (int j = 0; j < DV; j++) rk += (v[j] < v[i]) || (v[j] == v[i] && j < i);
-    if (rk == 10) med = v[i];
-  }
-  float den = med + 1e-6f;
-  for (int d = 0; d < DV; d++) norm[b*DV + d] = v[d] / den;
-}
-
-__global__ __launch_bounds__(256) void k_rank(const float* __restrict__ norm,
-    const float* __restrict__ thrv, float* __restrict__ stat){
-  int tid = threadIdx.x;
-  int cand = tid >> 4, part = tid & 15;
-  int idx = blockIdx.x*16 + cand;
-  float val = norm[idx];
-  int cnt = 0;
-  int j0 = part*336;
-  for (int j = j0; j < j0 + 336; ++j){
-    float v = norm[j];
-    cnt += (v < val) || (v == val && j < idx);
-  }
-  __shared__ int sc[16][17];
-  sc[cand][part] = cnt;
-  __syncthreads();
-  if (part == 0){
-    int rank = 0;
-    #pragma unroll
-    for (int i = 0; i < 16; i++) rank += sc[cand][i];
-    float q = thrv[0];
-    float pos = q * 5375.0f;
-    int i0 = (int)floorf(pos);
-    int i1 = (i0 + 1 > 5375) ? 5375 : i0 + 1;
-    if (rank == i0) stat[200] = val;
-    if (rank == i1) stat[201] = val;
-  }
-}
-
-__global__ __launch_bounds__(256) void k_maskgelu(float* __restrict__ zA, const float* __restrict__ norm,
-    const float* __restrict__ stat, const float* __restrict__ thrv,
-    const float* __restrict__ wdct, const float* __restrict__ bdct,
-    float* __restrict__ part){
-  int r = blockIdx.x, tid = threadIdx.x;
-  int d = r % DV, brow = r / DV;
-  float q = thrv[0];
-  float pos = q * 5375.0f; float f = pos - floorf(pos);
-  float thr = stat[200] + (stat[201] - stat[200]) * f;
-  float mask = norm[r] > thr ? 1.0f : 0.0f;
-  float w = wdct[d], b = bdct[d];
-  float s = 0.f, s2 = 0.f;
-  for (int i = tid; i < 512; i += 256){
-    float v = zA[(size_t)r*512 + i] * mask * w + b;
-    float g = gelu_f(v);
-    zA[(size_t)r*512 + i] = g;
-    s += g; s2 += g*g;
-  }
-  for (int off = 32; off; off >>= 1){ s += __shfl_down(s, off); s2 += __shfl_down(s2, off); }
-  __shared__ float wsum[4][2];
-  int wv = tid >> 6;
-  if ((tid & 63) == 0){ wsum[wv][0] = s; wsum[wv][1] = s2; }
-  __syncthreads();
-  if (tid == 0){
-    float S  = wsum[0][0]+wsum[1][0]+wsum[2][0]+wsum[3][0];
-    float S2 = wsum[0][1]+wsum[1][1]+wsum[2][1]+wsum[3][1];
-    part[(2*d)*256 + brow] = S;
-    part[(2*d+1)*256 + brow] = S2;
-  }
-}
-
-__global__ __launch_bounds__(256) void k_bnfin2(const float* __restrict__ part, int P,
-    const float* __restrict__ g, const float* __restrict__ b, float count, float* __restrict__ ab){
-  int c = blockIdx.x, tid = threadIdx.x;
-  const float* ps = part + (size_t)(2*c)*P;
-  const float* pq = part + (size_t)(2*c+1)*P;
-  float s = 0.f, s2 = 0.f;
-  for (int i = tid; i < P; i += 256){ s += ps[i]; s2 += pq[i]; }
-  for (int off = 32; off; off >>= 1){ s += __shfl_down(s, off); s2 += __shfl_down(s2, off); }
-  __shared__ float ws[4][2];
-  if ((tid & 63) == 0){ ws[tid>>6][0] = s; ws[tid>>6][1] = s2; }
-  __syncthreads();
-  if (tid == 0){
-    float S1 = ws[0][0]+ws[1][0]+ws[2][0]+ws[3][0];
-    float S2 = ws[0][1]+ws[1][1]+ws[2][1]+ws[3][1];
-    float mean = S1 / count;
-    float var  = S2 / count - mean*mean;
-    float al = g[c] * rsqrtf(var + 1e-5f);
-    float be = b[c] - mean * al;
-    ab[2*c] = al; ab[2*c+1] = be;
-  }
-}
-
-__global__ __launch_bounds__(256) void k_patch(const float* __restrict__ xt, const float* __restrict__ Tn,
-    const float* __restrict__ tb, float* __restrict__ t, float* __restrict__ part){
-  int blk = blockIdx.x, tid = threadIdx.x;
-  int n0 = tid >> 4, qq = tid & 15;
-  int n1 = n0 + 16;
-  float T0[16], T1[16];
-  #pragma unroll
-  for (int q2 = 0; q2 < 16; q2++){
-    T0[q2] = Tn[n0*256 + q2*16 + qq];
-    T1[q2] = Tn[n1*256 + q2*16 + qq];
-  }
-  float tb0 = tb[n0*16 + qq], tb1 = tb[n1*16 + qq];
-  float s0 = 0.f, q0 = 0.f, s1 = 0.f, q1 = 0.f;
-  #pragma unroll
-  for (int rr = 0; rr < 4; rr++){
-    int r = blk*4 + rr;
-    float x0 = xt[(size_t)r*512 + tid];
-    float x1 = xt[(size_t)r*512 + tid + 256];
-    float a0 = tb0, a1 = tb1;
-    #pragma unroll
-    for (int q2 = 0; q2 < 16; q2++){
-      a0 += __shfl(x0, q2, 16) * T0[q2];
-      a1 += __shfl(x1, q2, 16) * T1[q2];
-    }
-    t[(size_t)r*512 + tid] = a0;       s0 += a0; q0 += a0*a0;
-    t[(size_t)r*512 + tid + 256] = a1; s1 += a1; q1 += a1*a1;
-  }
-  #pragma unroll
-  for (int off = 1; off < 16; off <<= 1){
-    s0 += __shfl_xor(s0, off); q0 += __shfl_xor(q0, off);
-    s1 += __shfl_xor(s1, off); q1 += __shfl_xor(q1, off);
-  }
-  if (qq == 0){
-    part[(2*n0)*1344 + blk] = s0; part[(2*n0+1)*1344 + blk] = q0;
-    part[(2*n1)*1344 + blk] = s1; part[(2*n1+1)*1344 + blk] = q1;
-  }
-}
-
-__global__ __launch_bounds__(256) void k_z2(float* __restrict__ t, float* __restrict__ zcp,
-    const float* __restrict__ abp, const float* __restrict__ wdc1,
-    const float* __restrict__ bdc1, float* __restrict__ part){
-  int blk = blockIdx.x, tid = threadIdx.x;
-  int n0 = tid >> 4, qq = tid & 15;
-  int n1 = n0 + 16;
-  float al0 = abp[2*n0], be0 = abp[2*n0+1], al1 = abp[2*n1], be1 = abp[2*n1+1];
-  float w00 = wdc1[n0*3], w01 = wdc1[n0*3+1], w02 = wdc1[n0*3+2], bb0 = bdc1[n0];
-  float w10 = wdc1[n1*3], w11 = wdc1[n1*3+1], w12 = wdc1[n1*3+2], bb1 = bdc1[n1];
-  float s0 = 0.f, q0 = 0.f, s1 = 0.f, q1 = 0.f;
-  #pragma unroll
-  for (int rr = 0; rr < 4; rr++){
-    int r = blk*4 + rr;
-    float v0 = t[(size_t)r*512 + tid];
-    float v1 = t[(size_t)r*512 + tid + 256];
-    float z0  = gelu_f(al0*v0 + be0);
-    float z1v = gelu_f(al1*v1 + be1);
-    float l0 = __shfl_up(z0, 1, 16);    if (qq == 0)  l0 = 0.f;
-    float r0 = __shfl_down(z0, 1, 16);  if (qq == 15) r0 = 0.f;
-    float l1 = __shfl_up(z1v, 1, 16);   if (qq == 0)  l1 = 0.f;
-    float r1 = __shfl_down(z1v, 1, 16); if (qq == 15) r1 = 0.f;
-    float cv0 = w00*l0 + w01*z0  + w02*r0 + bb0;
-    float cv1 = w10*l1 + w11*z1v + w12*r1 + bb1;
-    zcp[(size_t)r*512 + tid] = cv0;       t[(size_t)r*512 + tid] = z0;
-    zcp[(size_t)r*512 + tid + 256] = cv1; t[(size_t)r*512 + tid + 256] = z1v;
-    s0 += cv0; q0 += cv0*cv0; s1 += cv1; q1 += cv1*cv1;
-  }
-  #pragma unroll
-  for (int off = 1; off < 16; off <<= 1){
-    s0 += __shfl_xor(s0, off); q0 += __shfl_xor(q0, off);
-    s1 += __shfl_xor(s1, off); q1 += __shfl_xor(q1, off);
-  }
-  if (qq == 0){
-    part[(2*n0)*1344 + blk] = s0; part[(2*n0+1)*1344 + blk] = q0;
-    part[(2*n1)*1344 + blk] = s1; part[(2*n1+1)*1344 + blk] = q1;
-  }
-}
-
 __global__ __launch_bounds__(256) void k_z2fatt(float* __restrict__ zcp, const float* __restrict__ z2,
     const float* __restrict__ ab, const float* __restrict__ z1,
     const float* __restrict__ dvec, float* __restrict__ att){
@@ -555,16 +590,6 @@
   for (int d = 0; d < DV; d++){ v[d] = expf(v[d] - mx); ss += v[d]; }
   float inv = 1.0f / ss;
   for (int d = 0; d < DV; d++) att1[b*DV + d] = v[d] * inv;
-}
-
-__global__ __launch_bounds__(256) void k_bcat(const float* __restrict__ Wm1, const float* __restrict__ M,
-                                              unsigned short* __restrict__ Bt){
-  int i = blockIdx.x*256 + threadIdx.x;
-  int c = i >> 9, m = i & 511;
-  float v = 0.f;
-  if (c < 96) v = Wm1[m*96 + c];
-  else if (c >= 128 && c < 224) v = M[m*96 + (c - 128)];
-  Bt[i] = (unsigned short)f2b(v);
 }
 
 __global__ __launch_bounds__(256) void k_out(const float* __restrict__ Hcat, const float* __restrict__ c,
@@ -628,39 +653,27 @@
   float* abdep= w + OFF_ABDEP;
   int*   flag = (int*)(w + OFF_FLAG);
   float* S    = w + OFF_STG;
+  float* tbuf = w + OFF_T;
+  float* partP = w + OFF_PARTP;
+  float* partD = w + OFF_PARTD;
+  float* e_part= w + OFF_EPART;
+  float* partM = w + OFF_PARTM;
+  unsigned short* BcatTh = (unsigned short*)(w + OFF_BCAT);
   float* Hcat = zA;
-  unsigned short* BcatTh = (unsigned short*)(zA + 1500000);
-  float* partA  = w + OFF_D2;
-  float* e_part = w + OFF_D3 + 131072;
-  float* partB  = w + OFF_D3 + 131072;
 
   Ptrs ptrs;
   for (int i = 0; i < 30; i++) ptrs.p[i] = d_in[i];
 
-  k_init<<<193, 256, 0, stream>>>((const unsigned*)d_in[13], stat, cb, Mb, flag);
-  k_stage<<<3338, 256, 0, stream>>>(ptrs, S, flag);
-  k_transpose<<<1024, 256, 0, stream>>>(d_in[0], xt, flag);
-  k_dctmats<<<1024, 256, 0, stream>>>(D2h, D2l, D3h, S, dvec);
-  k_foldM<<<dim3(192, 8), 256, 0, stream>>>(S, Mb);
-  k_foldC<<<128, 256, 0, stream>>>(S, cb);
-  k_foldTn<<<32, 256, 0, stream>>>(S, Tn, tb);
-
-  k_gemm0<<<dim3(8,84), 256, 0, stream>>>(xt, D2h, D2l, zA, e_part);
-  k_ered<<<21, 256, 0, stream>>>(e_part, en);
-  k_med<<<1, 256, 0, stream>>>(en, nrm);
-  k_rank<<<336, 256, 0, stream>>>(nrm, S+S_THR, stat);
-  k_maskgelu<<<NROW, 256, 0, stream>>>(zA, nrm, stat, S+S_THR, S+S_WDCT, S+S_BDCT, partA);
-  k_bnfin2<<<DV, 256, 0, stream>>>(partA, 256, S+S_GD, S+S_BDN, 131072.0f, abd);
+  k_setup<<<5579, 256, 0, stream>>>(ptrs, w, xt, D2h, D2l, D3h, dvec);
+  k_fold<<<1696, 256, 0, stream>>>(S, Mb, cb, Tn, tb);
+  k_mega<<<2528, 256, 0, stream>>>(xt, D2h, D2l, zA, e_part, flag, Tn, tb, tbuf, partP, S, Mb, BcatTh);
+  k_mid1<<<33, 256, 0, stream>>>(e_part, en, nrm, partP, S, abp);
+  k_mid2<<<1680, 256, 0, stream>>>(nrm, S, stat, tbuf, zcp, abp, partD);
+  k_mid3<<<NROW + NP, 256, 0, stream>>>(zA, nrm, stat, S, partM, partD, abdep);
+  k_mid4<<<DV, 256, 0, stream>>>(partM, S, abd);
   k_gemm_mf<1><<<dim3(8,84), 256, 0, stream>>>(zA, nullptr, D3h, z1, abd, xt, S+S_WDCT, S+S_BDCT, 512);
-
-  k_patch<<<NROW/4, 256, 0, stream>>>(xt, Tn, tb, zA, partA);
-  k_bnfin2<<<NP, 256, 0, stream>>>(partA, 1344, S+S_GP, S+S_BP, 86016.0f, abp);
-  k_z2<<<NROW/4, 256, 0, stream>>>(zA, zcp, abp, S+S_WDC1, S+S_BDC1, partB);
-  k_bnfin2<<<NP, 256, 0, stream>>>(partB, 1344, S+S_GDEP, S+S_BDEP, 86016.0f, abdep);
-  k_z2fatt<<<NROW, 256, 0, stream>>>(zcp, zA, abdep, z1, dvec, att);
+  k_z2fatt<<<NROW, 256, 0, stream>>>(zcp, tbuf, abdep, z1, dvec, att);
   k_attfin<<<1, 256, 0, stream>>>(att, S, att1);
-
-  k_bcat<<<512, 256, 0, stream>>>(S+S_WM1, Mb, BcatTh);
   k_gemm_mf<3><<<dim3(4,84), 256, 0, stream>>>(z1, zcp, BcatTh, Hcat, att1, xt, nullptr, nullptr, 256);
   k_out<<<NROW/16, 256, 0, stream>>>(Hcat, cb, S, d_out, flag);
 }
```

Measured after the change: 287.0 us. 10.0% less time.
